# Performance work log

Measured on AMD Instinct MI355X. Metric: run time of the kernel, lower is better.

## Reference

```python
import jax, jax.numpy as jnp
import numpy as np

G = 7          # grid_size
A = 2          # anchors_per_cell
C = 3          # num_classes
L_COORD, L_OBJ, L_NOOBJ, L_CLS = 5.0, 1.0, 0.5, 2.0


def setup_inputs() -> dict:
    key = jax.random.key(0)
    k0, k1, k2, k3, k4 = jax.random.split(key, 5)
    B, M = 32768, 20
    predictions = jax.random.normal(k0, (B, G, G, A, 5 + C), dtype=jnp.float32)
    xy1 = jax.random.uniform(k1, (B, M, 2), dtype=jnp.float32) * 0.8
    wh = jax.random.uniform(k2, (B, M, 2), dtype=jnp.float32) * 0.19 + 0.01
    target_boxes = jnp.concatenate([xy1, xy1 + wh], axis=-1)  # valid x1<x2, y1<y2
    target_labels = jax.random.randint(k3, (B, M), 0, C, dtype=jnp.int32)
    num_objs = jax.random.randint(k4, (B,), 0, M + 1, dtype=jnp.int32)
    anchors = jnp.array([[0.971, 1.7338], [3.4579, 5.1653]], dtype=jnp.float32)
    class_weights = jnp.array([1.0, 4.9, 4.8], dtype=jnp.float32)
    return dict(predictions=predictions, target_boxes=target_boxes,
                target_labels=target_labels, num_objs=num_objs,
                anchors=anchors, class_weights=class_weights)


def assign_targets(target_boxes, target_labels, num_objs, anchors, B):
    """Vectorized scatter-based replacement of the nested python assignment loop."""
    M = target_boxes.shape[1]
    x1, y1, x2, y2 = [target_boxes[..., i] for i in range(4)]  # (B,M)
    cx, cy = (x1 + x2) * 0.5, (y1 + y2) * 0.5
    w, h = x2 - x1, y2 - y1
    valid = (w > 0) & (h > 0) & (jnp.arange(M)[None, :] < num_objs[:, None])
    gi = jnp.clip(jnp.floor(cy * G).astype(jnp.int32), 0, G - 1)
    gj = jnp.clip(jnp.floor(cx * G).astype(jnp.int32), 0, G - 1)
    wg, hg = w * G, h * G
    # anchor matching IoU (width/height only), (B,M,A)
    inter = jnp.minimum(wg[..., None], anchors[:, 0]) * jnp.minimum(hg[..., None], anchors[:, 1])
    union = (wg * hg)[..., None] + anchors[:, 0] * anchors[:, 1] - inter
    best_a = jnp.argmax(inter / (union + 1e-6), axis=-1).astype(jnp.int32)  # first max = torch loop tie-break
    aw = anchors[best_a, 0]
    ah = anchors[best_a, 1]
    tx = cx * G - gj.astype(jnp.float32)
    ty = cy * G - gi.astype(jnp.float32)
    tw = jnp.log(jnp.clip(wg, 0.01, None) / (aw + 1e-6))
    th = jnp.log(jnp.clip(hg, 0.01, None) / (ah + 1e-6))
    tvals = jnp.stack([tx, ty, tw, th], axis=-1)  # (B,M,4)
    N = B * G * G * A
    bidx = jnp.arange(B, dtype=jnp.int32)[:, None]
    flat = ((bidx * G + gi) * G + gj) * A + best_a  # (B,M)
    flat = jnp.where(valid, flat, N)                # invalid -> dropped by scatter
    idx = flat.ravel()
    obj_mask = jnp.zeros((N,), jnp.float32).at[idx].set(1.0, mode='drop')
    target_bbox = jnp.zeros((N, 4), jnp.float32).at[idx].set(tvals.reshape(-1, 4), mode='drop')
    target_cls = jnp.zeros((N,), jnp.int32).at[idx].set(target_labels.ravel(), mode='drop')
    shape = (B, G, G, A)
    return obj_mask.reshape(shape), target_bbox.reshape(shape + (4,)), target_cls.reshape(shape)


def reference(predictions, target_boxes, target_labels, num_objs, anchors, class_weights):
    B = predictions.shape[0]
    pred_obj = predictions[..., 0]
    pred_bbox = predictions[..., 1:5]
    pred_cls = predictions[..., 5:]
    m, target_bbox, target_cls = assign_targets(target_boxes, target_labels, num_objs, anchors, B)
    sp = jax.nn.softplus
    # BCE-with-logits: target is 1 on obj cells, 0 on noobj cells
    loss_obj = jnp.sum(m * sp(-pred_obj))
    loss_noobj = jnp.sum((1.0 - m) * sp(pred_obj))
    # smooth L1 (beta=1), summed over obj cells
    d = pred_bbox - target_bbox
    ad = jnp.abs(d)
    sl1 = jnp.where(ad < 1.0, 0.5 * d * d, ad - 0.5)
    loss_bbox = jnp.sum(m[..., None] * sl1)
    # weighted cross entropy on obj cells
    logZ = jax.nn.logsumexpimport if False else jax.scipy.special.logsumexp(pred_cls, axis=-1)
    logit_t = jnp.take_along_axis(pred_cls, target_cls[..., None], axis=-1)[..., 0]
    loss_cls = jnp.sum(m * class_weights[target_cls] * (logZ - logit_t))
    num_pos = jnp.maximum(jnp.sum(m), 1.0)
    total = (L_COORD * loss_bbox + L_OBJ * loss_obj + L_NOOBJ * loss_noobj + L_CLS * loss_cls) / num_pos
    return total
```

## Files before the change

kernel.cpp:

```cpp
#include <hip/hip_runtime.h>


namespace {
constexpr int kG = 7;
constexpr int kA = 2;
constexpr int kM = 20;
constexpr int kCells = kG * kG * kA;
constexpr int kCh = 8;
constexpr int kNB = 16;
constexpr int kBlock = 256;
}

__device__ __forceinline__ float softplusf(float x) {
    return fmaxf(x, 0.0f) + log1pf(expf(-fabsf(x)));
}

__global__ __launch_bounds__(kBlock) void det_loss_main(
    const float* __restrict__ preds,
    const float* __restrict__ tboxes,
    const int* __restrict__ tlabels,
    const int* __restrict__ nobjs,
    const float* __restrict__ anchors,
    const float* __restrict__ cweights,
    float* __restrict__ partial,
    int B)
{
    __shared__ float4 s_tv[kNB * kM];
    __shared__ int    s_lab[kNB * kM];
    __shared__ short  s_cell[kNB * kM];
    __shared__ short  s_table[kNB * kCells];
    __shared__ int    s_nobj[kNB];
    __shared__ float  s_red[kBlock / 64][5];

    const int tid = threadIdx.x;
    const int b0 = blockIdx.x * kNB;

    const float a00 = anchors[0], a01 = anchors[1];
    const float a10 = anchors[2], a11 = anchors[3];
    const float cw0 = cweights[0], cw1 = cweights[1], cw2 = cweights[2];

    if (tid < kNB) {
        const int b = b0 + tid;
        s_nobj[tid] = (b < B) ? nobjs[b] : 0;
    }
    for (int k = tid; k < kNB * kCells; k += kBlock) s_table[k] = -1;
    __syncthreads();

    for (int j = tid; j < kNB * kM; j += kBlock) {
        const int bl = j / kM;
        const int m  = j - bl * kM;
        const int b  = b0 + bl;
        short cell = -1;
        float4 tv = make_float4(0.f, 0.f, 0.f, 0.f);
        int lab = 0;
        if (b < B) {
            const float4 box = ((const float4*)tboxes)[(size_t)b0 * kM + j];
            const float x1 = box.x, y1 = box.y, x2 = box.z, y2 = box.w;
            const float cx = (x1 + x2) * 0.5f, cy = (y1 + y2) * 0.5f;
            const float w = x2 - x1, h = y2 - y1;
            if (w > 0.f && h > 0.f && m < s_nobj[bl]) {
                const int gi = min(max((int)floorf(cy * (float)kG), 0), kG - 1);
                const int gj = min(max((int)floorf(cx * (float)kG), 0), kG - 1);
                const float wg = w * (float)kG, hg = h * (float)kG;
                const float i0 = fminf(wg, a00) * fminf(hg, a01);
                const float u0 = wg * hg + a00 * a01 - i0;
                const float r0 = i0 / (u0 + 1e-6f);
                const float i1 = fminf(wg, a10) * fminf(hg, a11);
                const float u1 = wg * hg + a10 * a11 - i1;
                const float r1 = i1 / (u1 + 1e-6f);
                const int a = (r1 > r0) ? 1 : 0;
                const float aw = a ? a10 : a00;
                const float ah = a ? a11 : a01;
                tv.x = cx * (float)kG - (float)gj;
                tv.y = cy * (float)kG - (float)gi;
                tv.z = logf(fmaxf(wg, 0.01f) / (aw + 1e-6f));
                tv.w = logf(fmaxf(hg, 0.01f) / (ah + 1e-6f));
                cell = (short)((gi * kG + gj) * kA + a);
                lab = tlabels[(size_t)b0 * kM + j];
            }
        }
        s_tv[j] = tv;
        s_lab[j] = lab;
        s_cell[j] = cell;
    }
    __syncthreads();

    if (tid < kNB) {
        const int base = tid * kM;
        for (int m = 0; m < kM; ++m) {
            const short c = s_cell[base + m];
            if (c >= 0) s_table[tid * kCells + c] = (short)(base + m);
        }
    }
    __syncthreads();

    float acc_obj = 0.f, acc_noobj = 0.f, acc_bbox = 0.f, acc_cls = 0.f;
    int npos = 0;
    const float4* __restrict__ p4 = (const float4*)preds;
    const long long cellbase = (long long)b0 * kCells;
    for (int i = tid; i < kNB * kCells; i += kBlock) {
        const int bl = i / kCells;
        if (b0 + bl >= B) break;
        const long long ci = (cellbase + i) * 2;
        const float4 p0 = p4[ci];
        const float4 p1 = p4[ci + 1];
        const float po = p0.x;
        const short j = s_table[i];
        if (j >= 0) {
            acc_obj += softplusf(-po);
            const float4 tv = s_tv[j];
            const float d0 = p0.y - tv.x;
            const float d1 = p0.z - tv.y;
            const float d2 = p0.w - tv.z;
            const float d3 = p1.x - tv.w;
            float ad;
            ad = fabsf(d0); acc_bbox += (ad < 1.f) ? 0.5f * d0 * d0 : ad - 0.5f;
            ad = fabsf(d1); acc_bbox += (ad < 1.f) ? 0.5f * d1 * d1 : ad - 0.5f;
            ad = fabsf(d2); acc_bbox += (ad < 1.f) ? 0.5f * d2 * d2 : ad - 0.5f;
            ad = fabsf(d3); acc_bbox += (ad < 1.f) ? 0.5f * d3 * d3 : ad - 0.5f;
            const int lab = s_lab[j];
            const float c0 = p1.y, c1 = p1.z, c2 = p1.w;
            const float mx = fmaxf(c0, fmaxf(c1, c2));
            const float lse = mx + logf(expf(c0 - mx) + expf(c1 - mx) + expf(c2 - mx));
            const float logit = (lab == 0) ? c0 : ((lab == 1) ? c1 : c2);
            const float cwv   = (lab == 0) ? cw0 : ((lab == 1) ? cw1 : cw2);
            acc_cls += cwv * (lse - logit);
            ++npos;
        } else {
            acc_noobj += softplusf(po);
        }
    }

    float vals[5] = {acc_obj, acc_noobj, acc_bbox, acc_cls, (float)npos};
    #pragma unroll
    for (int k = 0; k < 5; ++k) {
        float v = vals[k];
        #pragma unroll
        for (int off = 32; off > 0; off >>= 1) v += __shfl_down(v, off, 64);
        vals[k] = v;
    }
    const int wave = tid >> 6;
    const int lane = tid & 63;
    if (lane == 0) {
        #pragma unroll
        for (int k = 0; k < 5; ++k) s_red[wave][k] = vals[k];
    }
    __syncthreads();
    if (tid == 0) {
        const int nb = gridDim.x;
        #pragma unroll
        for (int k = 0; k < 5; ++k) {
            float t = 0.f;
            #pragma unroll
            for (int w = 0; w < kBlock / 64; ++w) t += s_red[w][k];
            partial[(size_t)k * nb + blockIdx.x] = t;
        }
    }
}

__global__ __launch_bounds__(kBlock) void det_loss_reduce(
    const float* __restrict__ partial, int nblocks, float* __restrict__ out)
{
    __shared__ float s_red[kBlock / 64][5];
    const int tid = threadIdx.x;
    float v[5] = {0.f, 0.f, 0.f, 0.f, 0.f};
    for (int i = tid; i < nblocks; i += kBlock) {
        #pragma unroll
        for (int k = 0; k < 5; ++k) v[k] += partial[(size_t)k * nblocks + i];
    }
    #pragma unroll
    for (int k = 0; k < 5; ++k) {
        float x = v[k];
        #pragma unroll
        for (int off = 32; off > 0; off >>= 1) x += __shfl_down(x, off, 64);
        v[k] = x;
    }
    const int wave = tid >> 6;
    const int lane = tid & 63;
    if (lane == 0) {
        #pragma unroll
        for (int k = 0; k < 5; ++k) s_red[wave][k] = v[k];
    }
    __syncthreads();
    if (tid == 0) {
        float t[5];
        #pragma unroll
        for (int k = 0; k < 5; ++k) {
            float s = 0.f;
            #pragma unroll
            for (int w = 0; w < kBlock / 64; ++w) s += s_red[w][k];
            t[k] = s;
        }
        const float npv = fmaxf(t[4], 1.0f);
        out[0] = (5.0f * t[2] + 1.0f * t[0] + 0.5f * t[1] + 2.0f * t[3]) / npv;
    }
}

extern "C" void kernel_launch(void* const* d_in, const int* in_sizes, int n_in,
                              void* d_out, int out_size, void* d_ws, size_t ws_size,
                              hipStream_t stream) {
    const float* preds    = (const float*)d_in[0];
    const float* tboxes   = (const float*)d_in[1];
    const int*   tlabels  = (const int*)d_in[2];
    const int*   nobjs    = (const int*)d_in[3];
    const float* anchors  = (const float*)d_in[4];
    const float* cweights = (const float*)d_in[5];
    float* out = (float*)d_out;
    float* partial = (float*)d_ws;

    const int B = in_sizes[0] / (kCells * kCh);
    const int blocks = (B + kNB - 1) / kNB;

    det_loss_main<<<blocks, kBlock, 0, stream>>>(
        preds, tboxes, tlabels, nobjs, anchors, cweights, partial, B);
    det_loss_reduce<<<1, kBlock, 0, stream>>>(partial, blocks, out);
}
```

Before: 179.9 us.

## Replace dense cell table with compact positive list and strided objectness pass

Drops the per-cell assignment table. Each target now decides whether it is the last writer for its cell, and the winners are collected into a compact positive list with a shared atomic counter. The dense pass reads only the objectness logit of every cell, using a strided scalar load, and applies noobj softplus everywhere. Positive cells are handled afterwards by subtracting their noobj term and loading full predictions only for them. It also uses fast exp/log intrinsics and raises the block to 32 batches with 448 threads. The trade-offs are a strided read of one float per 32-byte cell and slightly less precise transcendentals.

```diff
diff --git a/kernel.cpp b/kernel.cpp
--- a/kernel.cpp
+++ b/kernel.cpp
@@ -7,12 +7,14 @@
 constexpr int kM = 20;
 constexpr int kCells = kG * kG * kA;
 constexpr int kCh = 8;
-constexpr int kNB = 16;
-constexpr int kBlock = 256;
-}
-
-__device__ __forceinline__ float softplusf(float x) {
-    return fmaxf(x, 0.0f) + log1pf(expf(-fabsf(x)));
+constexpr int kNB = 32;
+constexpr int kBlock = 448;
+constexpr int kTgt = kNB * kM;
+constexpr int kIters = (kNB * kCells) / kBlock;
+}
+
+__device__ __forceinline__ float softplus_fast(float x) {
+    return fmaxf(x, 0.0f) + __logf(1.0f + __expf(-fabsf(x)));
 }
 
 __global__ __launch_bounds__(kBlock) void det_loss_main(
@@ -25,35 +27,32 @@
     float* __restrict__ partial,
     int B)
 {
-    __shared__ float4 s_tv[kNB * kM];
-    __shared__ int    s_lab[kNB * kM];
-    __shared__ short  s_cell[kNB * kM];
-    __shared__ short  s_table[kNB * kCells];
+    __shared__ float4 s_tv[kTgt];
+    __shared__ short  s_cell[kTgt];
+    __shared__ int    s_pos[kTgt];
     __shared__ int    s_nobj[kNB];
-    __shared__ float  s_red[kBlock / 64][5];
+    __shared__ int    s_npos;
+    __shared__ float  s_red[kBlock / 64][4];
 
     const int tid = threadIdx.x;
     const int b0 = blockIdx.x * kNB;
-
-    const float a00 = anchors[0], a01 = anchors[1];
-    const float a10 = anchors[2], a11 = anchors[3];
-    const float cw0 = cweights[0], cw1 = cweights[1], cw2 = cweights[2];
 
     if (tid < kNB) {
         const int b = b0 + tid;
         s_nobj[tid] = (b < B) ? nobjs[b] : 0;
     }
-    for (int k = tid; k < kNB * kCells; k += kBlock) s_table[k] = -1;
-    __syncthreads();
-
-    for (int j = tid; j < kNB * kM; j += kBlock) {
+    if (tid == 0) s_npos = 0;
+    __syncthreads();
+
+    const float a00 = anchors[0], a01 = anchors[1];
+    const float a10 = anchors[2], a11 = anchors[3];
+
+    for (int j = tid; j < kTgt; j += kBlock) {
         const int bl = j / kM;
         const int m  = j - bl * kM;
-        const int b  = b0 + bl;
         short cell = -1;
         float4 tv = make_float4(0.f, 0.f, 0.f, 0.f);
-        int lab = 0;
-        if (b < B) {
+        if (b0 + bl < B) {
             const float4 box = ((const float4*)tboxes)[(size_t)b0 * kM + j];
             const float x1 = box.x, y1 = box.y, x2 = box.z, y2 = box.w;
             const float cx = (x1 + x2) * 0.5f, cy = (y1 + y2) * 0.5f;
@@ -73,67 +72,77 @@
                 const float ah = a ? a11 : a01;
                 tv.x = cx * (float)kG - (float)gj;
                 tv.y = cy * (float)kG - (float)gi;
-                tv.z = logf(fmaxf(wg, 0.01f) / (aw + 1e-6f));
-                tv.w = logf(fmaxf(hg, 0.01f) / (ah + 1e-6f));
-                cell = (short)((gi * kG + gj) * kA + a);
-                lab = tlabels[(size_t)b0 * kM + j];
+                tv.z = __logf(fmaxf(wg, 0.01f) / (aw + 1e-6f));
+                tv.w = __logf(fmaxf(hg, 0.01f) / (ah + 1e-6f));
+                cell = (short)(bl * kCells + (gi * kG + gj) * kA + a);
             }
         }
+        s_cell[j] = cell;
         s_tv[j] = tv;
-        s_lab[j] = lab;
-        s_cell[j] = cell;
-    }
-    __syncthreads();
-
-    if (tid < kNB) {
-        const int base = tid * kM;
-        for (int m = 0; m < kM; ++m) {
-            const short c = s_cell[base + m];
-            if (c >= 0) s_table[tid * kCells + c] = (short)(base + m);
-        }
-    }
-    __syncthreads();
-
-    float acc_obj = 0.f, acc_noobj = 0.f, acc_bbox = 0.f, acc_cls = 0.f;
-    int npos = 0;
-    const float4* __restrict__ p4 = (const float4*)preds;
-    const long long cellbase = (long long)b0 * kCells;
-    for (int i = tid; i < kNB * kCells; i += kBlock) {
-        const int bl = i / kCells;
-        if (b0 + bl >= B) break;
-        const long long ci = (cellbase + i) * 2;
-        const float4 p0 = p4[ci];
-        const float4 p1 = p4[ci + 1];
-        const float po = p0.x;
-        const short j = s_table[i];
-        if (j >= 0) {
-            acc_obj += softplusf(-po);
-            const float4 tv = s_tv[j];
-            const float d0 = p0.y - tv.x;
-            const float d1 = p0.z - tv.y;
-            const float d2 = p0.w - tv.z;
-            const float d3 = p1.x - tv.w;
-            float ad;
-            ad = fabsf(d0); acc_bbox += (ad < 1.f) ? 0.5f * d0 * d0 : ad - 0.5f;
-            ad = fabsf(d1); acc_bbox += (ad < 1.f) ? 0.5f * d1 * d1 : ad - 0.5f;
-            ad = fabsf(d2); acc_bbox += (ad < 1.f) ? 0.5f * d2 * d2 : ad - 0.5f;
-            ad = fabsf(d3); acc_bbox += (ad < 1.f) ? 0.5f * d3 * d3 : ad - 0.5f;
-            const int lab = s_lab[j];
-            const float c0 = p1.y, c1 = p1.z, c2 = p1.w;
-            const float mx = fmaxf(c0, fmaxf(c1, c2));
-            const float lse = mx + logf(expf(c0 - mx) + expf(c1 - mx) + expf(c2 - mx));
-            const float logit = (lab == 0) ? c0 : ((lab == 1) ? c1 : c2);
-            const float cwv   = (lab == 0) ? cw0 : ((lab == 1) ? cw1 : cw2);
-            acc_cls += cwv * (lse - logit);
-            ++npos;
-        } else {
-            acc_noobj += softplusf(po);
-        }
-    }
-
-    float vals[5] = {acc_obj, acc_noobj, acc_bbox, acc_cls, (float)npos};
+    }
+    __syncthreads();
+
+    for (int j = tid; j < kTgt; j += kBlock) {
+        const short c = s_cell[j];
+        if (c >= 0) {
+            const int bl = j / kM;
+            const int m  = j - bl * kM;
+            bool win = true;
+            for (int m2 = m + 1; m2 < kM; ++m2) {
+                if (s_cell[bl * kM + m2] == c) { win = false; break; }
+            }
+            if (win) {
+                const int idx = atomicAdd(&s_npos, 1);
+                s_pos[idx] = (j << 16) | (int)c;
+            }
+        }
+    }
+    __syncthreads();
+
+    float accO = 0.f, accN = 0.f, accB = 0.f, accC = 0.f;
+    const float* __restrict__ pblk = preds + (size_t)b0 * kCells * kCh;
+    if (b0 + kNB <= B) {
+        #pragma unroll
+        for (int k = 0; k < kIters; ++k) {
+            const float po = pblk[(size_t)(tid + k * kBlock) * kCh];
+            accN += softplus_fast(po);
+        }
+    } else {
+        const int ncell = (B - b0) * kCells;
+        for (int i = tid; i < ncell; i += kBlock)
+            accN += softplus_fast(pblk[(size_t)i * kCh]);
+    }
+
+    const int np = s_npos;
+    const float cw0 = cweights[0], cw1 = cweights[1], cw2 = cweights[2];
+    for (int t = tid; t < np; t += kBlock) {
+        const int pk = s_pos[t];
+        const int j  = pk >> 16;
+        const int ci = pk & 0xFFFF;
+        const float4* pc = (const float4*)(pblk + (size_t)ci * kCh);
+        const float4 p0 = pc[0];
+        const float4 p1 = pc[1];
+        const float spp = softplus_fast(p0.x);
+        accN -= spp;
+        accO += spp - p0.x;
+        const float4 tv = s_tv[j];
+        float d, ad;
+        d = p0.y - tv.x; ad = fabsf(d); accB += (ad < 1.f) ? 0.5f * d * d : ad - 0.5f;
+        d = p0.z - tv.y; ad = fabsf(d); accB += (ad < 1.f) ? 0.5f * d * d : ad - 0.5f;
+        d = p0.w - tv.z; ad = fabsf(d); accB += (ad < 1.f) ? 0.5f * d * d : ad - 0.5f;
+        d = p1.x - tv.w; ad = fabsf(d); accB += (ad < 1.f) ? 0.5f * d * d : ad - 0.5f;
+        const int lab = tlabels[(size_t)b0 * kM + j];
+        const float c0 = p1.y, c1 = p1.z, c2 = p1.w;
+        const float mx = fmaxf(c0, fmaxf(c1, c2));
+        const float lse = mx + __logf(__expf(c0 - mx) + __expf(c1 - mx) + __expf(c2 - mx));
+        const float logit = (lab == 0) ? c0 : ((lab == 1) ? c1 : c2);
+        const float cwv   = (lab == 0) ? cw0 : ((lab == 1) ? cw1 : cw2);
+        accC += cwv * (lse - logit);
+    }
+
+    float vals[4] = {accO, accN, accB, accC};
     #pragma unroll
-    for (int k = 0; k < 5; ++k) {
+    for (int k = 0; k < 4; ++k) {
         float v = vals[k];
         #pragma unroll
         for (int off = 32; off > 0; off >>= 1) v += __shfl_down(v, off, 64);
@@ -143,28 +152,29 @@
     const int lane = tid & 63;
     if (lane == 0) {
         #pragma unroll
-        for (int k = 0; k < 5; ++k) s_red[wave][k] = vals[k];
+        for (int k = 0; k < 4; ++k) s_red[wave][k] = vals[k];
     }
     __syncthreads();
     if (tid == 0) {
         const int nb = gridDim.x;
         #pragma unroll
-        for (int k = 0; k < 5; ++k) {
+        for (int k = 0; k < 4; ++k) {
             float t = 0.f;
             #pragma unroll
             for (int w = 0; w < kBlock / 64; ++w) t += s_red[w][k];
             partial[(size_t)k * nb + blockIdx.x] = t;
         }
-    }
-}
-
-__global__ __launch_bounds__(kBlock) void det_loss_reduce(
+        partial[(size_t)4 * nb + blockIdx.x] = (float)np;
+    }
+}
+
+__global__ __launch_bounds__(256) void det_loss_reduce(
     const float* __restrict__ partial, int nblocks, float* __restrict__ out)
 {
-    __shared__ float s_red[kBlock / 64][5];
+    __shared__ float s_red[4][5];
     const int tid = threadIdx.x;
     float v[5] = {0.f, 0.f, 0.f, 0.f, 0.f};
-    for (int i = tid; i < nblocks; i += kBlock) {
+    for (int i = tid; i < nblocks; i += 256) {
         #pragma unroll
         for (int k = 0; k < 5; ++k) v[k] += partial[(size_t)k * nblocks + i];
     }
@@ -188,7 +198,7 @@
         for (int k = 0; k < 5; ++k) {
             float s = 0.f;
             #pragma unroll
-            for (int w = 0; w < kBlock / 64; ++w) s += s_red[w][k];
+            for (int w = 0; w < 4; ++w) s += s_red[w][k];
             t[k] = s;
         }
         const float npv = fmaxf(t[4], 1.0f);
@@ -213,5 +223,5 @@
 
     det_loss_main<<<blocks, kBlock, 0, stream>>>(
         preds, tboxes, tlabels, nobjs, anchors, cweights, partial, B);
-    det_loss_reduce<<<1, kBlock, 0, stream>>>(partial, blocks, out);
-}
+    det_loss_reduce<<<1, 256, 0, stream>>>(partial, blocks, out);
+}
```

Result: no change. 178.1 us (-1.0%).

## Map one thread per cell with 5 batches per block and parallel target assignment

Applied to the files above, without the earlier changes.

Restructures the main kernel so each 512-thread block handles 5 batch items and each thread processes exactly one cell with branchless masked math. The serial per-batch table fill is replaced by a parallel last-writer-wins check among each batch's targets. Fast intrinsics (__expf/__logf) replace precise math, class weights are pre-gathered into shared memory, and partials are written as interleaved float4s reduced by a 1024-thread final kernel. This raises the block count considerably and adds per-block setup and reduction overhead, while the fast intrinsics can slightly change numerics.

```diff
diff --git a/kernel.cpp b/kernel.cpp
--- a/kernel.cpp
+++ b/kernel.cpp
@@ -7,12 +7,14 @@
 constexpr int kM = 20;
 constexpr int kCells = kG * kG * kA;
 constexpr int kCh = 8;
-constexpr int kNB = 16;
-constexpr int kBlock = 256;
-}
-
-__device__ __forceinline__ float softplusf(float x) {
-    return fmaxf(x, 0.0f) + log1pf(expf(-fabsf(x)));
+constexpr int kNBatch = 5;
+constexpr int kBlock = 512;
+constexpr int kTgtB = kNBatch * kM;
+constexpr int kCellsB = kNBatch * kCells;
+}
+
+__device__ __forceinline__ float softplus_fast(float x) {
+    return fmaxf(x, 0.0f) + __logf(1.0f + __expf(-fabsf(x)));
 }
 
 __global__ __launch_bounds__(kBlock) void det_loss_main(
@@ -25,40 +27,41 @@
     float* __restrict__ partial,
     int B)
 {
-    __shared__ float4 s_tv[kNB * kM];
-    __shared__ int    s_lab[kNB * kM];
-    __shared__ short  s_cell[kNB * kM];
-    __shared__ short  s_table[kNB * kCells];
-    __shared__ int    s_nobj[kNB];
+    __shared__ float4 s_tv[kTgtB + 1];
+    __shared__ float  s_cw[kTgtB + 1];
+    __shared__ int    s_lab[kTgtB + 1];
+    __shared__ short  s_cell[kTgtB];
+    __shared__ short  s_table[kCellsB];
     __shared__ float  s_red[kBlock / 64][5];
 
     const int tid = threadIdx.x;
-    const int b0 = blockIdx.x * kNB;
+    const int b0 = blockIdx.x * kNBatch;
+    const int nAct = min(kNBatch, B - b0) * kCells;
+
+    if (tid < kCellsB) s_table[tid] = -1;
+    if (tid == kBlock - 1) {
+        s_tv[kTgtB] = make_float4(0.f, 0.f, 0.f, 0.f);
+        s_cw[kTgtB] = 0.f;
+        s_lab[kTgtB] = 0;
+    }
 
     const float a00 = anchors[0], a01 = anchors[1];
     const float a10 = anchors[2], a11 = anchors[3];
-    const float cw0 = cweights[0], cw1 = cweights[1], cw2 = cweights[2];
-
-    if (tid < kNB) {
-        const int b = b0 + tid;
-        s_nobj[tid] = (b < B) ? nobjs[b] : 0;
-    }
-    for (int k = tid; k < kNB * kCells; k += kBlock) s_table[k] = -1;
-    __syncthreads();
-
-    for (int j = tid; j < kNB * kM; j += kBlock) {
-        const int bl = j / kM;
-        const int m  = j - bl * kM;
+
+    if (tid < kTgtB) {
+        const int bl = tid / kM;
+        const int m  = tid - bl * kM;
         const int b  = b0 + bl;
         short cell = -1;
         float4 tv = make_float4(0.f, 0.f, 0.f, 0.f);
+        float cwv = 0.f;
         int lab = 0;
-        if (b < B) {
-            const float4 box = ((const float4*)tboxes)[(size_t)b0 * kM + j];
+        if (b < B && m < nobjs[b]) {
+            const float4 box = ((const float4*)tboxes)[(size_t)b * kM + m];
             const float x1 = box.x, y1 = box.y, x2 = box.z, y2 = box.w;
             const float cx = (x1 + x2) * 0.5f, cy = (y1 + y2) * 0.5f;
             const float w = x2 - x1, h = y2 - y1;
-            if (w > 0.f && h > 0.f && m < s_nobj[bl]) {
+            if (w > 0.f && h > 0.f) {
                 const int gi = min(max((int)floorf(cy * (float)kG), 0), kG - 1);
                 const int gj = min(max((int)floorf(cx * (float)kG), 0), kG - 1);
                 const float wg = w * (float)kG, hg = h * (float)kG;
@@ -73,65 +76,69 @@
                 const float ah = a ? a11 : a01;
                 tv.x = cx * (float)kG - (float)gj;
                 tv.y = cy * (float)kG - (float)gi;
-                tv.z = logf(fmaxf(wg, 0.01f) / (aw + 1e-6f));
-                tv.w = logf(fmaxf(hg, 0.01f) / (ah + 1e-6f));
-                cell = (short)((gi * kG + gj) * kA + a);
-                lab = tlabels[(size_t)b0 * kM + j];
+                tv.z = __logf(fmaxf(wg, 0.01f) / (aw + 1e-6f));
+                tv.w = __logf(fmaxf(hg, 0.01f) / (ah + 1e-6f));
+                cell = (short)(bl * kCells + (gi * kG + gj) * kA + a);
+                lab = tlabels[(size_t)b * kM + m];
+                cwv = cweights[lab];
             }
         }
-        s_tv[j] = tv;
-        s_lab[j] = lab;
-        s_cell[j] = cell;
-    }
-    __syncthreads();
-
-    if (tid < kNB) {
-        const int base = tid * kM;
-        for (int m = 0; m < kM; ++m) {
-            const short c = s_cell[base + m];
-            if (c >= 0) s_table[tid * kCells + c] = (short)(base + m);
-        }
-    }
-    __syncthreads();
-
-    float acc_obj = 0.f, acc_noobj = 0.f, acc_bbox = 0.f, acc_cls = 0.f;
-    int npos = 0;
-    const float4* __restrict__ p4 = (const float4*)preds;
-    const long long cellbase = (long long)b0 * kCells;
-    for (int i = tid; i < kNB * kCells; i += kBlock) {
-        const int bl = i / kCells;
-        if (b0 + bl >= B) break;
-        const long long ci = (cellbase + i) * 2;
-        const float4 p0 = p4[ci];
-        const float4 p1 = p4[ci + 1];
+        s_cell[tid] = cell;
+        s_tv[tid] = tv;
+        s_cw[tid] = cwv;
+        s_lab[tid] = lab;
+    }
+    __syncthreads();
+
+    if (tid < kTgtB) {
+        const short c = s_cell[tid];
+        if (c >= 0) {
+            const int bl = tid / kM;
+            const int m  = tid - bl * kM;
+            bool win = true;
+            for (int m2 = m + 1; m2 < kM; ++m2) {
+                if (s_cell[bl * kM + m2] == c) { win = false; break; }
+            }
+            if (win) s_table[c] = (short)tid;
+        }
+    }
+    __syncthreads();
+
+    float accO = 0.f, accN = 0.f, accB = 0.f, accC = 0.f, npf = 0.f;
+    if (tid < nAct) {
+        const float4* __restrict__ pc =
+            (const float4*)preds + ((size_t)b0 * kCells + tid) * 2;
+        const float4 p0 = pc[0];
+        const float4 p1 = pc[1];
+        const int j = s_table[tid];
+        const bool pos = (j >= 0);
+        const int jj = pos ? j : kTgtB;
+        const float m = pos ? 1.f : 0.f;
+        const float4 tv = s_tv[jj];
+        const float cwv = s_cw[jj];
+        const int lab = s_lab[jj];
+
         const float po = p0.x;
-        const short j = s_table[i];
-        if (j >= 0) {
-            acc_obj += softplusf(-po);
-            const float4 tv = s_tv[j];
-            const float d0 = p0.y - tv.x;
-            const float d1 = p0.z - tv.y;
-            const float d2 = p0.w - tv.z;
-            const float d3 = p1.x - tv.w;
-            float ad;
-            ad = fabsf(d0); acc_bbox += (ad < 1.f) ? 0.5f * d0 * d0 : ad - 0.5f;
-            ad = fabsf(d1); acc_bbox += (ad < 1.f) ? 0.5f * d1 * d1 : ad - 0.5f;
-            ad = fabsf(d2); acc_bbox += (ad < 1.f) ? 0.5f * d2 * d2 : ad - 0.5f;
-            ad = fabsf(d3); acc_bbox += (ad < 1.f) ? 0.5f * d3 * d3 : ad - 0.5f;
-            const int lab = s_lab[j];
-            const float c0 = p1.y, c1 = p1.z, c2 = p1.w;
-            const float mx = fmaxf(c0, fmaxf(c1, c2));
-            const float lse = mx + logf(expf(c0 - mx) + expf(c1 - mx) + expf(c2 - mx));
-            const float logit = (lab == 0) ? c0 : ((lab == 1) ? c1 : c2);
-            const float cwv   = (lab == 0) ? cw0 : ((lab == 1) ? cw1 : cw2);
-            acc_cls += cwv * (lse - logit);
-            ++npos;
-        } else {
-            acc_noobj += softplusf(po);
-        }
-    }
-
-    float vals[5] = {acc_obj, acc_noobj, acc_bbox, acc_cls, (float)npos};
+        const float spo = softplus_fast(po);
+        accN = spo - m * spo;
+        accO = m * (spo - po);
+
+        float d, ad, sb;
+        d = p0.y - tv.x; ad = fabsf(d); sb  = (ad < 1.f) ? 0.5f * d * d : ad - 0.5f;
+        d = p0.z - tv.y; ad = fabsf(d); sb += (ad < 1.f) ? 0.5f * d * d : ad - 0.5f;
+        d = p0.w - tv.z; ad = fabsf(d); sb += (ad < 1.f) ? 0.5f * d * d : ad - 0.5f;
+        d = p1.x - tv.w; ad = fabsf(d); sb += (ad < 1.f) ? 0.5f * d * d : ad - 0.5f;
+        accB = m * sb;
+
+        const float c0 = p1.y, c1 = p1.z, c2 = p1.w;
+        const float mx = fmaxf(c0, fmaxf(c1, c2));
+        const float lse = mx + __logf(__expf(c0 - mx) + __expf(c1 - mx) + __expf(c2 - mx));
+        const float logit = (lab == 0) ? c0 : ((lab == 1) ? c1 : c2);
+        accC = m * cwv * (lse - logit);
+        npf = m;
+    }
+
+    float vals[5] = {accO, accN, accB, accC, npf};
     #pragma unroll
     for (int k = 0; k < 5; ++k) {
         float v = vals[k];
@@ -144,42 +151,6 @@
     if (lane == 0) {
         #pragma unroll
         for (int k = 0; k < 5; ++k) s_red[wave][k] = vals[k];
-    }
-    __syncthreads();
-    if (tid == 0) {
-        const int nb = gridDim.x;
-        #pragma unroll
-        for (int k = 0; k < 5; ++k) {
-            float t = 0.f;
-            #pragma unroll
-            for (int w = 0; w < kBlock / 64; ++w) t += s_red[w][k];
-            partial[(size_t)k * nb + blockIdx.x] = t;
-        }
-    }
-}
-
-__global__ __launch_bounds__(kBlock) void det_loss_reduce(
-    const float* __restrict__ partial, int nblocks, float* __restrict__ out)
-{
-    __shared__ float s_red[kBlock / 64][5];
-    const int tid = threadIdx.x;
-    float v[5] = {0.f, 0.f, 0.f, 0.f, 0.f};
-    for (int i = tid; i < nblocks; i += kBlock) {
-        #pragma unroll
-        for (int k = 0; k < 5; ++k) v[k] += partial[(size_t)k * nblocks + i];
-    }
-    #pragma unroll
-    for (int k = 0; k < 5; ++k) {
-        float x = v[k];
-        #pragma unroll
-        for (int off = 32; off > 0; off >>= 1) x += __shfl_down(x, off, 64);
-        v[k] = x;
-    }
-    const int wave = tid >> 6;
-    const int lane = tid & 63;
-    if (lane == 0) {
-        #pragma unroll
-        for (int k = 0; k < 5; ++k) s_red[wave][k] = v[k];
     }
     __syncthreads();
     if (tid == 0) {
@@ -189,6 +160,47 @@
             float s = 0.f;
             #pragma unroll
             for (int w = 0; w < kBlock / 64; ++w) s += s_red[w][k];
+            t[k] = s;
+        }
+        float4* p4o = (float4*)(partial + (size_t)blockIdx.x * 8);
+        p4o[0] = make_float4(t[0], t[1], t[2], t[3]);
+        p4o[1] = make_float4(t[4], 0.f, 0.f, 0.f);
+    }
+}
+
+__global__ __launch_bounds__(1024) void det_loss_reduce(
+    const float* __restrict__ partial, int nblocks, float* __restrict__ out)
+{
+    __shared__ float s_red[16][5];
+    const int tid = threadIdx.x;
+    const float4* __restrict__ p4 = (const float4*)partial;
+    float v[5] = {0.f, 0.f, 0.f, 0.f, 0.f};
+    for (int e = tid; e < nblocks; e += 1024) {
+        const float4 a = p4[2 * e];
+        const float4 b = p4[2 * e + 1];
+        v[0] += a.x; v[1] += a.y; v[2] += a.z; v[3] += a.w; v[4] += b.x;
+    }
+    #pragma unroll
+    for (int k = 0; k < 5; ++k) {
+        float x = v[k];
+        #pragma unroll
+        for (int off = 32; off > 0; off >>= 1) x += __shfl_down(x, off, 64);
+        v[k] = x;
+    }
+    const int wave = tid >> 6;
+    const int lane = tid & 63;
+    if (lane == 0) {
+        #pragma unroll
+        for (int k = 0; k < 5; ++k) s_red[wave][k] = v[k];
+    }
+    __syncthreads();
+    if (tid == 0) {
+        float t[5];
+        #pragma unroll
+        for (int k = 0; k < 5; ++k) {
+            float s = 0.f;
+            #pragma unroll
+            for (int w = 0; w < 16; ++w) s += s_red[w][k];
             t[k] = s;
         }
         const float npv = fmaxf(t[4], 1.0f);
@@ -209,9 +221,9 @@
     float* partial = (float*)d_ws;
 
     const int B = in_sizes[0] / (kCells * kCh);
-    const int blocks = (B + kNB - 1) / kNB;
+    const int blocks = (B + kNBatch - 1) / kNBatch;
 
     det_loss_main<<<blocks, kBlock, 0, stream>>>(
         preds, tboxes, tlabels, nobjs, anchors, cweights, partial, B);
-    det_loss_reduce<<<1, kBlock, 0, stream>>>(partial, blocks, out);
-}
+    det_loss_reduce<<<1, 1024, 0, stream>>>(partial, blocks, out);
+}
```

Result: slower. 188.4 us (+4.7%).
